# Performance work log

Hardware: AMD Instinct MI355X
Metric: run time of the kernel (lower is better)

The kernel has to match this reference:

```python
import jax, jax.numpy as jnp
import numpy as np

B, N, D, H, T = 2048, 128, 256, 8, 64
HD = D // H
TANH_C = 10.0
MASK_PENALTY = 1e9


def setup_inputs() -> dict:
    key = jax.random.key(0)
    ks = jax.random.split(key, 16)
    s = 1.0 / np.sqrt(D).astype(np.float32)
    w = lambda k: jax.random.normal(k, (D, D), jnp.float32) * s
    return {
        'node_emb': jax.random.normal(ks[0], (B, N, D), jnp.float32),
        'graph_emb': jax.random.normal(ks[1], (B, D), jnp.float32),
        'W_target': w(ks[2]), 'W_global': w(ks[3]),
        'W_K1': w(ks[4]), 'W_K2': w(ks[5]),
        'W_Q': w(ks[6]), 'W_V': w(ks[7]),
        'Wq_m': w(ks[8]), 'Wk_m': w(ks[9]), 'Wv_m': w(ks[10]), 'Wo_m': w(ks[11]),
        'targets': jax.random.randint(ks[12], (T, B), 0, N, jnp.int32),
        'masks': jax.random.randint(ks[13], (T, B, N), 0, 2, jnp.int32),
    }


def _mha(q, k, v, Wq, Wk, Wv, Wo):
    # q: [B,1,D]; k,v: [B,N,D]. Standard multi-head attention (glimpse).
    qh = (q @ Wq.T).reshape(B, 1, H, HD).transpose(0, 2, 1, 3)   # [B,H,1,HD]
    kh = (k @ Wk.T).reshape(B, N, H, HD).transpose(0, 2, 1, 3)   # [B,H,N,HD]
    vh = (v @ Wv.T).reshape(B, N, H, HD).transpose(0, 2, 1, 3)
    scores = jnp.einsum('bhqd,bhnd->bhqn', qh, kh) / np.sqrt(HD).astype(np.float32)
    attn = jax.nn.softmax(scores, axis=-1)
    out = jnp.einsum('bhqn,bhnd->bhqd', attn, vh)                # [B,H,1,HD]
    out = out.transpose(0, 2, 1, 3).reshape(B, 1, D)
    return out @ Wo.T


def reference(node_emb, graph_emb, W_target, W_global, W_K1, W_K2, W_Q, W_V,
              Wq_m, Wk_m, Wv_m, Wo_m, targets, masks):
    # Step-invariant projections (embeddings fixed across decode steps here).
    keys = node_emb @ W_K1.T      # [B,N,D]
    vals = node_emb @ W_V.T       # [B,N,D]
    key2 = node_emb @ W_K2.T      # [B,N,D]
    g_ctx = graph_emb @ W_global.T  # [B,D]
    inv_sqrt_d = np.float32(1.0 / np.sqrt(D))

    def step(ll, tm):
        tgt, mask = tm  # tgt:[B] int32, mask:[B,N] int32
        tgt_emb = jnp.take_along_axis(node_emb, tgt[:, None, None], axis=1)[:, 0, :]  # [B,D]
        context = (tgt_emb @ W_target.T + g_ctx)[:, None, :]      # [B,1,D]
        glimpse = _mha(context, keys, vals, Wq_m, Wk_m, Wv_m, Wo_m)  # [B,1,D]
        query = glimpse @ W_Q.T                                    # [B,1,D]
        logits = jnp.einsum('bqd,bnd->bn', query, key2) * inv_sqrt_d  # [B,N]
        logits = TANH_C * jnp.tanh(logits) - mask.astype(jnp.float32) * MASK_PENALTY
        log_p = jax.nn.log_softmax(logits, axis=1)
        actions = jnp.argmax(log_p, axis=1)                        # greedy TopKSampler
        ll = ll + jnp.take_along_axis(log_p, actions[:, None], axis=1)[:, 0]
        return ll, None

    ll, _ = jax.lax.scan(step, jnp.zeros(B, jnp.float32), (targets, masks))
    return ll
```

## Files before the change

### kernel.cpp

```cpp
#include <hip/hip_runtime.h>
#include <hip/hip_bf16.h>

#define BB 2048
#define NN 128
#define DD 256
#define HH 8
#define TT 64

typedef __bf16 bf16x8 __attribute__((ext_vector_type(8)));
typedef float f32x4 __attribute__((ext_vector_type(4)));

static __device__ __forceinline__ f32x4 mfma16(bf16x8 a, bf16x8 b, f32x4 c) {
  return __builtin_amdgcn_mfma_f32_16x16x32_bf16(a, b, c, 0, 0, 0);
}

static __device__ __forceinline__ f32x4 zero4() {
  f32x4 z = {0.f, 0.f, 0.f, 0.f};
  return z;
}

static __device__ __forceinline__ bf16x8 cvt8(const float* p) {
  const float4 x0 = *(const float4*)p;
  const float4 x1 = *(const float4*)(p + 4);
  bf16x8 r;
  r[0] = (__bf16)x0.x; r[1] = (__bf16)x0.y; r[2] = (__bf16)x0.z; r[3] = (__bf16)x0.w;
  r[4] = (__bf16)x1.x; r[5] = (__bf16)x1.y; r[6] = (__bf16)x1.z; r[7] = (__bf16)x1.w;
  return r;
}

static __device__ __forceinline__ unsigned pk2(float a, float b) {
  __bf16 x = (__bf16)a, y = (__bf16)b;
  unsigned short ux, uy;
  __builtin_memcpy(&ux, &x, 2);
  __builtin_memcpy(&uy, &y, 2);
  return (unsigned)ux | ((unsigned)uy << 16);
}

static __device__ __forceinline__ float fast_tanh10(float y) {
  const float e = __expf(2.f * y);
  return 10.f - 20.f * __builtin_amdgcn_rcpf(1.f + e);
}

__global__ void fold1(const float* __restrict__ Wq_m, const float* __restrict__ W_target,
                      const float* __restrict__ W_global, const float* __restrict__ Wk_m,
                      const float* __restrict__ W_K1, const float* __restrict__ Wv_m,
                      const float* __restrict__ W_V, const float* __restrict__ W_Q,
                      const float* __restrict__ Wo_m,
                      __bf16* __restrict__ WTQ, float* __restrict__ WGQT,
                      __bf16* __restrict__ WKH, __bf16* __restrict__ WVH,
                      float* __restrict__ WQO) {
  const int p = blockIdx.x >> 8;
  const int i = blockIdx.x & 255;
  const int t = threadIdx.x;
  __shared__ float arow[256];
  const float* A;
  const float* Bm;
  if (p == 0)      { A = Wq_m; Bm = W_target; }
  else if (p == 1) { A = Wq_m; Bm = W_global; }
  else if (p == 2) { A = Wk_m; Bm = W_K1; }
  else if (p == 3) { A = Wv_m; Bm = W_V; }
  else             { A = W_Q;  Bm = Wo_m; }
  arow[t] = A[i * 256 + t];
  __syncthreads();
  float acc = 0.f;
  for (int k = 0; k < 256; ++k) acc = fmaf(arow[k], Bm[k * 256 + t], acc);
  if (p == 0)      WTQ[i * 256 + t] = (__bf16)acc;
  else if (p == 1) WGQT[t * 256 + i] = acc;
  else if (p == 2) WKH[i * 256 + t] = (__bf16)acc;
  else if (p == 3) WVH[i * 256 + t] = (__bf16)acc;
  else             WQO[i * 256 + t] = acc;
}

__global__ void fold2(const float* __restrict__ WQO, const float* __restrict__ W_K2,
                      __bf16* __restrict__ WZL) {
  const int j = blockIdx.x;
  const int t = threadIdx.x;
  __shared__ float col[256];
  col[t] = W_K2[t * 256 + j];
  __syncthreads();
  float acc = 0.f;
  for (int d = 0; d < 256; ++d) acc = fmaf(WQO[d * 256 + t], col[d], acc);
  WZL[j * 256 + t] = (__bf16)acc;
}

__global__ void gq_kernel(const float* __restrict__ ge, const float* __restrict__ WGQT,
                          float* __restrict__ GQ) {
  const int b0 = blockIdx.x * 8;
  const int t = threadIdx.x;
  __shared__ float g[8][256];
#pragma unroll
  for (int i = 0; i < 8; ++i) g[i][t] = ge[(b0 + i) * 256 + t];
  __syncthreads();
  float acc[8] = {0.f, 0.f, 0.f, 0.f, 0.f, 0.f, 0.f, 0.f};
  for (int j = 0; j < 256; ++j) {
    const float wv = WGQT[j * 256 + t];
#pragma unroll
    for (int i = 0; i < 8; ++i) acc[i] = fmaf(wv, g[i][j], acc[i]);
  }
#pragma unroll
  for (int i = 0; i < 8; ++i) GQ[(b0 + i) * 256 + t] = acc[i];
}

__global__ __launch_bounds__(512)
void kvq_kernel(const float* __restrict__ E, const int* __restrict__ tg,
                const __bf16* __restrict__ WKH, const __bf16* __restrict__ WVH,
                const __bf16* __restrict__ WTQ, const float* __restrict__ GQ,
                __bf16* __restrict__ KH, __bf16* __restrict__ VT,
                __bf16* __restrict__ Qb) {
  const int b = blockIdx.x;
  const int tid = threadIdx.x;
  const int w = tid >> 6;
  const int l = tid & 63;
  const int lr = l & 15;
  const int lg = l >> 4;
  __shared__ __align__(16) __bf16 Es[128 * 264];
  __shared__ int tgs[64];
  if (tid < 64) tgs[tid] = tg[tid * BB + b];
  const float* Eb = E + (size_t)b * NN * DD;
#pragma unroll
  for (int it = 0; it < 8; ++it) {
    const int c = it * 512 + tid;
    const int row = c >> 5;
    const int c8 = c & 31;
    *(bf16x8*)&Es[row * 264 + c8 * 8] = cvt8(Eb + row * 256 + c8 * 8);
  }
  __syncthreads();

  {
    f32x4 acc[8][2];
#pragma unroll
    for (int mf = 0; mf < 8; ++mf)
#pragma unroll
      for (int nf = 0; nf < 2; ++nf) acc[mf][nf] = zero4();
    for (int kk = 0; kk < 8; ++kk) {
      bf16x8 aF[8], bF[2];
#pragma unroll
      for (int mf = 0; mf < 8; ++mf)
        aF[mf] = *(const bf16x8*)&Es[(mf * 16 + lr) * 264 + kk * 32 + lg * 8];
#pragma unroll
      for (int nf = 0; nf < 2; ++nf)
        bF[nf] = *(const bf16x8*)(WKH + (size_t)(w * 32 + nf * 16 + lr) * DD + kk * 32 + lg * 8);
#pragma unroll
      for (int mf = 0; mf < 8; ++mf)
#pragma unroll
        for (int nf = 0; nf < 2; ++nf) acc[mf][nf] = mfma16(aF[mf], bF[nf], acc[mf][nf]);
    }
    __bf16* KHb = KH + (size_t)b * NN * DD;
#pragma unroll
    for (int mf = 0; mf < 8; ++mf)
#pragma unroll
      for (int nf = 0; nf < 2; ++nf)
#pragma unroll
        for (int r = 0; r < 4; ++r)
          KHb[(mf * 16 + lg * 4 + r) * DD + w * 32 + nf * 16 + lr] = (__bf16)acc[mf][nf][r];
  }

  {
    f32x4 acc[2][8];
#pragma unroll
    for (int mf = 0; mf < 2; ++mf)
#pragma unroll
      for (int nf = 0; nf < 8; ++nf) acc[mf][nf] = zero4();
    for (int kk = 0; kk < 8; ++kk) {
      bf16x8 aW[2], bE[8];
#pragma unroll
      for (int mf = 0; mf < 2; ++mf)
        aW[mf] = *(const bf16x8*)(WVH + (size_t)(w * 32 + mf * 16 + lr) * DD + kk * 32 + lg * 8);
#pragma unroll
      for (int nf = 0; nf < 8; ++nf)
        bE[nf] = *(const bf16x8*)&Es[(nf * 16 + lr) * 264 + kk * 32 + lg * 8];
#pragma unroll
      for (int mf = 0; mf < 2; ++mf)
#pragma unroll
        for (int nf = 0; nf < 8; ++nf) acc[mf][nf] = mfma16(aW[mf], bE[nf], acc[mf][nf]);
    }
    __bf16* VTb = VT + (size_t)b * DD * NN;
#pragma unroll
    for (int mf = 0; mf < 2; ++mf)
#pragma unroll
      for (int nf = 0; nf < 8; ++nf)
#pragma unroll
        for (int r = 0; r < 4; ++r)
          VTb[(w * 32 + mf * 16 + lg * 4 + r) * NN + nf * 16 + lr] = (__bf16)acc[mf][nf][r];
  }

  {
    f32x4 acc[4][2];
#pragma unroll
    for (int mf = 0; mf < 4; ++mf)
#pragma unroll
      for (int nf = 0; nf < 2; ++nf) acc[mf][nf] = zero4();
    int rowoff[4];
#pragma unroll
    for (int mf = 0; mf < 4; ++mf) rowoff[mf] = tgs[mf * 16 + lr] * 264;
    for (int kk = 0; kk < 8; ++kk) {
      bf16x8 aF[4], bF[2];
#pragma unroll
      for (int mf = 0; mf < 4; ++mf)
        aF[mf] = *(const bf16x8*)&Es[rowoff[mf] + kk * 32 + lg * 8];
#pragma unroll
      for (int nf = 0; nf < 2; ++nf)
        bF[nf] = *(const bf16x8*)(WTQ + (size_t)(w * 32 + nf * 16 + lr) * DD + kk * 32 + lg * 8);
#pragma unroll
      for (int mf = 0; mf < 4; ++mf)
#pragma unroll
        for (int nf = 0; nf < 2; ++nf) acc[mf][nf] = mfma16(aF[mf], bF[nf], acc[mf][nf]);
    }
#pragma unroll
    for (int nf = 0; nf < 2; ++nf) {
      const int col = w * 32 + nf * 16 + lr;
      const float g = GQ[b * DD + col];
#pragma unroll
      for (int mf = 0; mf < 4; ++mf)
#pragma unroll
        for (int r = 0; r < 4; ++r)
          Qb[((size_t)b * TT + mf * 16 + lg * 4 + r) * DD + col] = (__bf16)(acc[mf][nf][r] + g);
    }
  }
}

__global__ __launch_bounds__(256)
void attn4_kernel(const __bf16* __restrict__ Qb, const __bf16* __restrict__ KH,
                  const __bf16* __restrict__ VT, __bf16* __restrict__ HO) {
  const int j = (blockIdx.x & 7) * ((BB * 4) / 8) + (blockIdx.x >> 3);
  const int b = j >> 2;
  const int c0 = (j & 3) * 64;
  const int tid = threadIdx.x;
  const int w = tid >> 6;
  const int l = tid & 63;
  const int lr = l & 15;
  const int lg = l >> 4;
  const int T0 = w * 16;

  __shared__ __align__(16) __bf16 KHs[128 * 72];
  __shared__ __align__(16) __bf16 VTs[64 * 136];
  __shared__ __align__(16) __bf16 Ps[4][16 * 136];

  const __bf16* KHb = KH + (size_t)b * NN * DD;
  const __bf16* VTb = VT + (size_t)b * DD * NN;

  bf16x8 aq[2];
#pragma unroll
  for (int h = 0; h < 2; ++h)
    aq[h] = *(const bf16x8*)(Qb + ((size_t)b * TT + T0 + lr) * DD + c0 + h * 32 + lg * 8);

#pragma unroll
  for (int it = 0; it < 4; ++it) {
    const int c = it * 256 + tid;
    const int row = c >> 3;
    const int c8 = c & 7;
    *(bf16x8*)&KHs[row * 72 + c8 * 8] = *(const bf16x8*)(KHb + (size_t)row * DD + c0 + c8 * 8);
  }
#pragma unroll
  for (int it = 0; it < 4; ++it) {
    const int c = it * 256 + tid;
    const int row = c >> 4;
    const int c8 = c & 15;
    *(bf16x8*)&VTs[row * 136 + c8 * 8] =
        *(const bf16x8*)(VTb + (size_t)(c0 + row) * NN + c8 * 8);
  }
  __syncthreads();

  __bf16* myp = Ps[w];
  __bf16* HOb = HO + (size_t)b * TT * DD + c0;

#pragma unroll
  for (int h = 0; h < 2; ++h) {
    f32x4 s[8];
#pragma unroll
    for (int nf = 0; nf < 8; ++nf)
      s[nf] = mfma16(*(const bf16x8*)&KHs[(nf * 16 + lr) * 72 + h * 32 + lg * 8], aq[h], zero4());

    float mx = -1e30f;
#pragma unroll
    for (int nf = 0; nf < 8; ++nf)
#pragma unroll
      for (int r = 0; r < 4; ++r) mx = fmaxf(mx, s[nf][r]);
    mx = fmaxf(mx, __shfl_xor(mx, 16));
    mx = fmaxf(mx, __shfl_xor(mx, 32));

    float sm = 0.f;
    uint2 evp[8];
#pragma unroll
    for (int nf = 0; nf < 8; ++nf) {
      const float e0 = __expf((s[nf][0] - mx) * 0.17677669529663687f);
      const float e1 = __expf((s[nf][1] - mx) * 0.17677669529663687f);
      const float e2 = __expf((s[nf][2] - mx) * 0.17677669529663687f);
      const float e3 = __expf((s[nf][3] - mx) * 0.17677669529663687f);
      sm += (e0 + e1) + (e2 + e3);
      evp[nf].x = pk2(e0, e1);
      evp[nf].y = pk2(e2, e3);
    }
    sm += __shfl_xor(sm, 16);
    sm += __shfl_xor(sm, 32);

#pragma unroll
    for (int nf = 0; nf < 8; ++nf)
      *(uint2*)&myp[lr * 136 + nf * 16 + lg * 4] = evp[nf];

    f32x4 o0 = zero4(), o1 = zero4();
#pragma unroll
    for (int kk = 0; kk < 4; ++kk) {
      const bf16x8 ap = *(const bf16x8*)&myp[lr * 136 + kk * 32 + lg * 8];
      o0 = mfma16(ap, *(const bf16x8*)&VTs[(h * 32 + lr) * 136 + kk * 32 + lg * 8], o0);
      o1 = mfma16(ap, *(const bf16x8*)&VTs[(h * 32 + 16 + lr) * 136 + kk * 32 + lg * 8], o1);
    }
#pragma unroll
    for (int r = 0; r < 4; ++r) {
      const float inv = __builtin_amdgcn_rcpf(__shfl(sm, lg * 4 + r));
      HOb[(size_t)(T0 + lg * 4 + r) * DD + h * 32 + lr] = (__bf16)(o0[r] * inv);
      HOb[(size_t)(T0 + lg * 4 + r) * DD + h * 32 + 16 + lr] = (__bf16)(o1[r] * inv);
    }
  }
}

__global__ __launch_bounds__(256)
void zlog2_kernel(const float* __restrict__ E, const __bf16* __restrict__ HO,
                  const __bf16* __restrict__ WZL, const int* __restrict__ MK,
                  float* __restrict__ out) {
  const int b = blockIdx.x;
  const int tid = threadIdx.x;
  const int w = tid >> 6;
  const int l = tid & 63;
  const int lr = l & 15;
  const int lg = l >> 4;
  const int T0 = w * 16;
  __shared__ __align__(16) __bf16 Zs[64 * 264];
  __shared__ float red[4];

  const float* Eb = E + (size_t)b * NN * DD;
  const __bf16* HOb = HO + (size_t)b * TT * DD;

  {
    f32x4 acc[4][4];
#pragma unroll
    for (int mf = 0; mf < 4; ++mf)
#pragma unroll
      for (int nf = 0; nf < 4; ++nf) acc[mf][nf] = zero4();
    for (int kk = 0; kk < 8; ++kk) {
      bf16x8 aF[4], bF[4];
#pragma unroll
      for (int mf = 0; mf < 4; ++mf)
        aF[mf] = *(const bf16x8*)(HOb + (size_t)(mf * 16 + lr) * DD + kk * 32 + lg * 8);
#pragma unroll
      for (int nf = 0; nf < 4; ++nf)
        bF[nf] = *(const bf16x8*)(WZL + (size_t)(w * 64 + nf * 16 + lr) * DD + kk * 32 + lg * 8);
#pragma unroll
      for (int mf = 0; mf < 4; ++mf)
#pragma unroll
        for (int nf = 0; nf < 4; ++nf) acc[mf][nf] = mfma16(aF[mf], bF[nf], acc[mf][nf]);
    }
#pragma unroll
    for (int mf = 0; mf < 4; ++mf)
#pragma unroll
      for (int nf = 0; nf < 4; ++nf)
#pragma unroll
        for (int r = 0; r < 4; ++r)
          Zs[(mf * 16 + lg * 4 + r) * 264 + w * 64 + nf * 16 + lr] = (__bf16)acc[mf][nf][r];
  }
  __syncthreads();

  {
    f32x4 sa[8];
#pragma unroll
    for (int nf = 0; nf < 8; ++nf) sa[nf] = zero4();
    for (int kk = 0; kk < 8; ++kk) {
      const bf16x8 bZ = *(const bf16x8*)&Zs[(T0 + lr) * 264 + kk * 32 + lg * 8];
#pragma unroll
      for (int nf = 0; nf < 8; ++nf) {
        const bf16x8 aE = cvt8(Eb + (size_t)(nf * 16 + lr) * DD + kk * 32 + lg * 8);
        sa[nf] = mfma16(aE, bZ, sa[nf]);
      }
    }
    const int t = T0 + lr;
    float xs[8][4];
    float mx = -3e38f;
#pragma unroll
    for (int nf = 0; nf < 8; ++nf) {
      const int4 mk4 = *(const int4*)(MK + ((size_t)t * BB + b) * NN + nf * 16 + lg * 4);
      xs[nf][0] = fast_tanh10(sa[nf][0] * 0.0625f) - (float)mk4.x * 1e9f;
      xs[nf][1] = fast_tanh10(sa[nf][1] * 0.0625f) - (float)mk4.y * 1e9f;
      xs[nf][2] = fast_tanh10(sa[nf][2] * 0.0625f) - (float)mk4.z * 1e9f;
      xs[nf][3] = fast_tanh10(sa[nf][3] * 0.0625f) - (float)mk4.w * 1e9f;
      mx = fmaxf(mx, fmaxf(fmaxf(xs[nf][0], xs[nf][1]), fmaxf(xs[nf][2], xs[nf][3])));
    }
    mx = fmaxf(mx, __shfl_xor(mx, 16));
    mx = fmaxf(mx, __shfl_xor(mx, 32));
    float sm = 0.f;
#pragma unroll
    for (int nf = 0; nf < 8; ++nf)
#pragma unroll
      for (int r = 0; r < 4; ++r) sm += __expf(xs[nf][r] - mx);
    sm += __shfl_xor(sm, 16);
    sm += __shfl_xor(sm, 32);
    float part = logf(sm);
    part += __shfl_xor(part, 1);
    part += __shfl_xor(part, 2);
    part += __shfl_xor(part, 4);
    part += __shfl_xor(part, 8);
    if (l == 0) red[w] = part;
  }
  __syncthreads();
  if (tid == 0) out[b] = -(red[0] + red[1] + red[2] + red[3]);
}

extern "C" void kernel_launch(void* const* d_in, const int* in_sizes, int n_in,
                              void* d_out, int out_size, void* d_ws, size_t ws_size,
                              hipStream_t stream) {
  (void)in_sizes; (void)n_in; (void)out_size; (void)ws_size;
  const float* node_emb  = (const float*)d_in[0];
  const float* graph_emb = (const float*)d_in[1];
  const float* W_target  = (const float*)d_in[2];
  const float* W_global  = (const float*)d_in[3];
  const float* W_K1      = (const float*)d_in[4];
  const float* W_K2      = (const float*)d_in[5];
  const float* W_Q       = (const float*)d_in[6];
  const float* W_V       = (const float*)d_in[7];
  const float* Wq_m      = (const float*)d_in[8];
  const float* Wk_m      = (const float*)d_in[9];
  const float* Wv_m      = (const float*)d_in[10];
  const float* Wo_m      = (const float*)d_in[11];
  const int* targets     = (const int*)d_in[12];
  const int* masks       = (const int*)d_in[13];

  char* p = (char*)d_ws;
  __bf16* KH  = (__bf16*)p; p += (size_t)BB * NN * DD * 2;
  __bf16* VT  = (__bf16*)p; p += (size_t)BB * DD * NN * 2;
  __bf16* HO  = (__bf16*)p; p += (size_t)BB * TT * DD * 2;
  __bf16* Qb  = (__bf16*)p; p += (size_t)BB * TT * DD * 2;
  __bf16* WTQ = (__bf16*)p; p += 256 * 256 * 2;
  __bf16* WKH = (__bf16*)p; p += 256 * 256 * 2;
  __bf16* WVH = (__bf16*)p; p += 256 * 256 * 2;
  __bf16* WZL = (__bf16*)p; p += 256 * 256 * 2;
  float* WGQT = (float*)p;  p += 256 * 256 * 4;
  float* WQO  = (float*)p;  p += 256 * 256 * 4;
  float* GQ   = (float*)p;  p += (size_t)BB * DD * 4;

  fold1<<<1280, 256, 0, stream>>>(Wq_m, W_target, W_global, Wk_m, W_K1, Wv_m, W_V, W_Q, Wo_m,
                                  WTQ, WGQT, WKH, WVH, WQO);
  fold2<<<256, 256, 0, stream>>>(WQO, W_K2, WZL);
  gq_kernel<<<BB / 8, 256, 0, stream>>>(graph_emb, WGQT, GQ);
  kvq_kernel<<<BB, 512, 0, stream>>>(node_emb, targets, WKH, WVH, WTQ, GQ, KH, VT, Qb);
  attn4_kernel<<<BB * 4, 256, 0, stream>>>(Qb, KH, VT, HO);
  zlog2_kernel<<<BB, 256, 0, stream>>>(node_emb, HO, WZL, masks, (float*)d_out);
}
```

Measured before the change: 499.9 us.

## Move target-query projection from kv kernel into attention kernel

The kv kernel no longer computes the per-step query projection. Instead it writes the gathered bf16 target embeddings to a workspace buffer. The attention kernel computes the query slice for its head group with MFMA from those embeddings and WTQ, adds the graph term, and stages the result through shared memory. This shortens the kv kernel and spreads the query GEMM across the attention blocks. In exchange, each of the four column-group blocks per batch re-reads the gathered embeddings, and the query math now sits in front of the attention work.

```diff
diff --git a/kernel.cpp b/kernel.cpp
--- a/kernel.cpp
+++ b/kernel.cpp
@@ -102,11 +102,10 @@
 }
 
 __global__ __launch_bounds__(512)
-void kvq_kernel(const float* __restrict__ E, const int* __restrict__ tg,
-                const __bf16* __restrict__ WKH, const __bf16* __restrict__ WVH,
-                const __bf16* __restrict__ WTQ, const float* __restrict__ GQ,
-                __bf16* __restrict__ KH, __bf16* __restrict__ VT,
-                __bf16* __restrict__ Qb) {
+void kv_kernel(const float* __restrict__ E, const int* __restrict__ tg,
+               const __bf16* __restrict__ WKH, const __bf16* __restrict__ WVH,
+               __bf16* __restrict__ KH, __bf16* __restrict__ VT,
+               __bf16* __restrict__ Eg) {
   const int b = blockIdx.x;
   const int tid = threadIdx.x;
   const int w = tid >> 6;
@@ -127,6 +126,17 @@
   __syncthreads();
 
   {
+    __bf16* Egb = Eg + (size_t)b * TT * DD;
+#pragma unroll
+    for (int it = 0; it < 4; ++it) {
+      const int c = it * 512 + tid;
+      const int row = c >> 5;
+      const int c8 = c & 31;
+      *(bf16x8*)(Egb + row * 256 + c8 * 8) = *(const bf16x8*)&Es[tgs[row] * 264 + c8 * 8];
+    }
+  }
+
+  {
     f32x4 acc[8][2];
 #pragma unroll
     for (int mf = 0; mf < 8; ++mf)
@@ -183,44 +193,11 @@
         for (int r = 0; r < 4; ++r)
           VTb[(w * 32 + mf * 16 + lg * 4 + r) * NN + nf * 16 + lr] = (__bf16)acc[mf][nf][r];
   }
-
-  {
-    f32x4 acc[4][2];
-#pragma unroll
-    for (int mf = 0; mf < 4; ++mf)
-#pragma unroll
-      for (int nf = 0; nf < 2; ++nf) acc[mf][nf] = zero4();
-    int rowoff[4];
-#pragma unroll
-    for (int mf = 0; mf < 4; ++mf) rowoff[mf] = tgs[mf * 16 + lr] * 264;
-    for (int kk = 0; kk < 8; ++kk) {
-      bf16x8 aF[4], bF[2];
-#pragma unroll
-      for (int mf = 0; mf < 4; ++mf)
-        aF[mf] = *(const bf16x8*)&Es[rowoff[mf] + kk * 32 + lg * 8];
-#pragma unroll
-      for (int nf = 0; nf < 2; ++nf)
-        bF[nf] = *(const bf16x8*)(WTQ + (size_t)(w * 32 + nf * 16 + lr) * DD + kk * 32 + lg * 8);
-#pragma unroll
-      for (int mf = 0; mf < 4; ++mf)
-#pragma unroll
-        for (int nf = 0; nf < 2; ++nf) acc[mf][nf] = mfma16(aF[mf], bF[nf], acc[mf][nf]);
-    }
-#pragma unroll
-    for (int nf = 0; nf < 2; ++nf) {
-      const int col = w * 32 + nf * 16 + lr;
-      const float g = GQ[b * DD + col];
-#pragma unroll
-      for (int mf = 0; mf < 4; ++mf)
-#pragma unroll
-        for (int r = 0; r < 4; ++r)
-          Qb[((size_t)b * TT + mf * 16 + lg * 4 + r) * DD + col] = (__bf16)(acc[mf][nf][r] + g);
-    }
-  }
 }
 
 __global__ __launch_bounds__(256)
-void attn4_kernel(const __bf16* __restrict__ Qb, const __bf16* __restrict__ KH,
+void attn6_kernel(const __bf16* __restrict__ Eg, const __bf16* __restrict__ WTQ,
+                  const float* __restrict__ GQ, const __bf16* __restrict__ KH,
                   const __bf16* __restrict__ VT, __bf16* __restrict__ HO) {
   const int j = (blockIdx.x & 7) * ((BB * 4) / 8) + (blockIdx.x >> 3);
   const int b = j >> 2;
@@ -236,13 +213,10 @@
   __shared__ __align__(16) __bf16 VTs[64 * 136];
   __shared__ __align__(16) __bf16 Ps[4][16 * 136];
 
+  const __bf16* Egb = Eg + (size_t)b * TT * DD;
   const __bf16* KHb = KH + (size_t)b * NN * DD;
   const __bf16* VTb = VT + (size_t)b * DD * NN;
-
-  bf16x8 aq[2];
-#pragma unroll
-  for (int h = 0; h < 2; ++h)
-    aq[h] = *(const bf16x8*)(Qb + ((size_t)b * TT + T0 + lr) * DD + c0 + h * 32 + lg * 8);
+  __bf16* myp = Ps[w];
 
 #pragma unroll
   for (int it = 0; it < 4; ++it) {
@@ -259,9 +233,31 @@
     *(bf16x8*)&VTs[row * 136 + c8 * 8] =
         *(const bf16x8*)(VTb + (size_t)(c0 + row) * NN + c8 * 8);
   }
-  __syncthreads();
-
-  __bf16* myp = Ps[w];
+
+  {
+    f32x4 qa[4] = {zero4(), zero4(), zero4(), zero4()};
+    for (int kk = 0; kk < 8; ++kk) {
+      const bf16x8 aF = *(const bf16x8*)(Egb + (size_t)(T0 + lr) * DD + kk * 32 + lg * 8);
+#pragma unroll
+      for (int nf = 0; nf < 4; ++nf) {
+        const bf16x8 bF =
+            *(const bf16x8*)(WTQ + (size_t)(c0 + nf * 16 + lr) * DD + kk * 32 + lg * 8);
+        qa[nf] = mfma16(aF, bF, qa[nf]);
+      }
+    }
+#pragma unroll
+    for (int nf = 0; nf < 4; ++nf) {
+      const float g = GQ[b * DD + c0 + nf * 16 + lr];
+#pragma unroll
+      for (int r = 0; r < 4; ++r)
+        myp[(lg * 4 + r) * 72 + nf * 16 + lr] = (__bf16)(qa[nf][r] + g);
+    }
+  }
+  bf16x8 aq[2];
+#pragma unroll
+  for (int h = 0; h < 2; ++h) aq[h] = *(const bf16x8*)&myp[lr * 72 + h * 32 + lg * 8];
+  __syncthreads();
+
   __bf16* HOb = HO + (size_t)b * TT * DD + c0;
 
 #pragma unroll
@@ -427,7 +423,7 @@
   __bf16* KH  = (__bf16*)p; p += (size_t)BB * NN * DD * 2;
   __bf16* VT  = (__bf16*)p; p += (size_t)BB * DD * NN * 2;
   __bf16* HO  = (__bf16*)p; p += (size_t)BB * TT * DD * 2;
-  __bf16* Qb  = (__bf16*)p; p += (size_t)BB * TT * DD * 2;
+  __bf16* Eg  = (__bf16*)p; p += (size_t)BB * TT * DD * 2;
   __bf16* WTQ = (__bf16*)p; p += 256 * 256 * 2;
   __bf16* WKH = (__bf16*)p; p += 256 * 256 * 2;
   __bf16* WVH = (__bf16*)p; p += 256 * 256 * 2;
@@ -440,7 +436,7 @@
                                   WTQ, WGQT, WKH, WVH, WQO);
   fold2<<<256, 256, 0, stream>>>(WQO, W_K2, WZL);
   gq_kernel<<<BB / 8, 256, 0, stream>>>(graph_emb, WGQT, GQ);
-  kvq_kernel<<<BB, 512, 0, stream>>>(node_emb, targets, WKH, WVH, WTQ, GQ, KH, VT, Qb);
-  attn4_kernel<<<BB * 4, 256, 0, stream>>>(Qb, KH, VT, HO);
+  kv_kernel<<<BB, 512, 0, stream>>>(node_emb, targets, WKH, WVH, KH, VT, Eg);
+  attn6_kernel<<<BB * 4, 256, 0, stream>>>(Eg, WTQ, GQ, KH, VT, HO);
   zlog2_kernel<<<BB, 256, 0, stream>>>(node_emb, HO, WZL, masks, (float*)d_out);
 }
```

New measurement: 597.6 us. +19.5%, slower.
